# Performance work log

Measured on AMD Instinct MI355X. Metric: run time of the kernel, lower is better.

The kernel has to match this reference:

```python
import jax, jax.numpy as jnp
import numpy as np

B, C, H, W = 8, 512, 64, 64
RED = 8
D = C // RED  # query/key channels


def setup_inputs() -> dict:
    key = jax.random.key(0)
    ks = jax.random.split(key, 5)
    skip = jax.random.normal(ks[0], (B, C, H, W), dtype=jnp.float32)
    res = jax.random.normal(ks[1], (B, C, H, W), dtype=jnp.float32)
    # 1x1 Conv1d weights (no bias). Spectral norm is a weight parametrization;
    # these tensors represent the effective (normalized) weights at forward time.
    Wq = jax.random.normal(ks[2], (D, C), dtype=jnp.float32) * 0.02
    Wk = jax.random.normal(ks[3], (D, C), dtype=jnp.float32) * 0.02
    Wv = jax.random.normal(ks[4], (C, C), dtype=jnp.float32) * 0.02
    gamma = jnp.asarray([0.5], dtype=jnp.float32)  # nonzero so attention branch contributes
    return {"skip": skip, "res": res, "Wq": Wq, "Wk": Wk, "Wv": Wv, "gamma": gamma}


def reference(skip, res, Wq, Wk, Wv, gamma):
    b, c, h, w = skip.shape
    n = h * w
    x_skip = skip.reshape(b, c, n)  # [B, C, N]
    x_res = res.reshape(b, c, n)
    # 1x1 convs == per-position matmuls
    f = jnp.einsum('dc,bcn->bdn', Wq, x_skip)  # [B, D, N]
    g = jnp.einsum('dc,bcn->bdn', Wk, x_skip)  # [B, D, N]
    hv = jnp.einsum('oc,bcn->bon', Wv, x_res)  # [B, C, N]
    # scores[b, i, j] = sum_d f[b, d, i] * g[b, d, j]; softmax over dim=1 (the i axis)
    scores = jnp.einsum('bdi,bdj->bij', f, g)  # [B, N, N]
    beta = jax.nn.softmax(scores, axis=1)
    o = gamma * jnp.einsum('bci,bij->bcj', hv, beta) + x_skip  # [B, C, N]
    return o.reshape(b, c, h, w)
```

## Files before the change

kernel.cpp:

```cpp
#include <hip/hip_runtime.h>


#define B_ 8
#define C_ 512
#define N_ 4096
#define D_ 64

typedef __bf16 bf16x8 __attribute__((ext_vector_type(8)));
typedef float  f32x16 __attribute__((ext_vector_type(16)));

#define MFMA32 __builtin_amdgcn_mfma_f32_32x32x16_bf16

__device__ __forceinline__ unsigned pk_bf16(float a, float b) {
  unsigned r;
  asm("v_cvt_pk_bf16_f32 %0, %1, %2" : "=v"(r) : "v"(a), "v"(b));
  return r;
}

__device__ __forceinline__ bf16x8 ldg_frag(const unsigned short* p) {
  uint4 u = *(const uint4*)p;
  return __builtin_bit_cast(bf16x8, u);
}
__device__ __forceinline__ bf16x8 lds_frag(const unsigned char* p) {
  uint4 u = *(const uint4*)p;
  return __builtin_bit_cast(bf16x8, u);
}

__global__ void cvt_w(const float* __restrict__ src, unsigned short* __restrict__ dst, int n) {
  int i = (blockIdx.x * blockDim.x + threadIdx.x) * 2;
  if (i + 1 < n + 1) {
    unsigned v = pk_bf16(src[i], src[i + 1]);
    *(unsigned*)(dst + i) = v;
  }
}

__device__ __forceinline__ void stage64(const float* __restrict__ src,
                                        unsigned char* __restrict__ dst, int t) {
  int si = (t & 15) << 2;
  int cl = (t >> 4) << 1;
#pragma unroll
  for (int p = 0; p < 2; ++p) {
    int c = cl + p * 32;
    const float* r0 = src + (size_t)c * N_ + si;
    float4 a0 = *(const float4*)r0;
    float4 a1 = *(const float4*)(r0 + N_);
    const float* f0 = (const float*)&a0;
    const float* f1 = (const float*)&a1;
    int cb = c << 1;
#pragma unroll
    for (int k = 0; k < 4; ++k) {
      int ii = si + k;
      unsigned v = pk_bf16(f0[k], f1[k]);
      *(unsigned*)(dst + (((ii << 7) + cb) ^ ((ii & 7) << 4))) = v;
    }
  }
}

__global__ __launch_bounds__(256, 2) void fg_proj(
    const float* __restrict__ skip,
    const unsigned short* __restrict__ Wqb, const unsigned short* __restrict__ Wkb,
    unsigned short* __restrict__ Kmat, unsigned short* __restrict__ Qmat) {
  __shared__ __align__(16) unsigned char Xs[2][8192];
  int blk = blockIdx.x, b = blk & 7, i0 = (blk >> 3) << 6;
  int t = threadIdx.x, lane = t & 63, w = t >> 6, hi = lane >> 5, l5 = lane & 31;
  int dh = w >> 1, ih = w & 1;
  f32x16 ka, qa;
#pragma unroll
  for (int r = 0; r < 16; ++r) { ka[r] = 0.f; qa[r] = 0.f; }
  int il = (ih << 5) + l5;
  int dr = (dh << 5) + l5;
#pragma unroll 1
  for (int kk = 0; kk < 8; ++kk) {
    int c0 = kk << 6;
    unsigned char* buf = Xs[kk & 1];
    stage64(skip + ((size_t)(b * C_ + c0)) * N_ + i0, buf, t);
    __syncthreads();
#pragma unroll
    for (int ks = 0; ks < 4; ++ks) {
      int co = (ks << 4) + (hi << 3);
      bf16x8 aq = ldg_frag(Wqb + (size_t)dr * C_ + c0 + co);
      bf16x8 ak = ldg_frag(Wkb + (size_t)dr * C_ + c0 + co);
      bf16x8 bx = lds_frag(buf + (((il << 7) + (co << 1)) ^ ((il & 7) << 4)));
      ka = MFMA32(aq, bx, ka, 0, 0, 0);
      qa = MFMA32(ak, bx, qa, 0, 0, 0);
    }
  }
  size_t rowb = ((size_t)b * N_ + i0 + il) * D_ + (dh << 5);
#pragma unroll
  for (int q = 0; q < 4; ++q) {
    int dq = (q << 3) + (hi << 2);
    uint2 v;
    v.x = pk_bf16(ka[q * 4 + 0], ka[q * 4 + 1]);
    v.y = pk_bf16(ka[q * 4 + 2], ka[q * 4 + 3]);
    *(uint2*)(Kmat + rowb + dq) = v;
    v.x = pk_bf16(qa[q * 4 + 0], qa[q * 4 + 1]);
    v.y = pk_bf16(qa[q * 4 + 2], qa[q * 4 + 3]);
    *(uint2*)(Qmat + rowb + dq) = v;
  }
}

__global__ __launch_bounds__(256, 2) void hv_proj(
    const float* __restrict__ res, const unsigned short* __restrict__ Wvb,
    unsigned short* __restrict__ Vmat) {
  __shared__ __align__(16) unsigned char Xs[2][8192];
  int blk = blockIdx.x, b = blk & 7, i0 = (blk >> 3) << 6;
  int t = threadIdx.x, lane = t & 63, w = t >> 6, hi = lane >> 5, l5 = lane & 31;
  int cw = w << 7;
  f32x16 acc[2][4];
#pragma unroll
  for (int a = 0; a < 2; ++a)
#pragma unroll
    for (int c = 0; c < 4; ++c)
#pragma unroll
      for (int r = 0; r < 16; ++r) acc[a][c][r] = 0.f;
#pragma unroll 1
  for (int kk = 0; kk < 8; ++kk) {
    int c0 = kk << 6;
    unsigned char* buf = Xs[kk & 1];
    stage64(res + ((size_t)(b * C_ + c0)) * N_ + i0, buf, t);
    __syncthreads();
#pragma unroll
    for (int ks = 0; ks < 4; ++ks) {
      int co = (ks << 4) + (hi << 3);
      bf16x8 a0 = lds_frag(buf + (((l5 << 7) + (co << 1)) ^ ((l5 & 7) << 4)));
      bf16x8 a1 = lds_frag(buf + ((((32 + l5) << 7) + (co << 1)) ^ ((l5 & 7) << 4)));
#pragma unroll
      for (int ct = 0; ct < 4; ++ct) {
        bf16x8 bv = ldg_frag(Wvb + (size_t)(cw + (ct << 5) + l5) * C_ + c0 + co);
        acc[0][ct] = MFMA32(a0, bv, acc[0][ct], 0, 0, 0);
        acc[1][ct] = MFMA32(a1, bv, acc[1][ct], 0, 0, 0);
      }
    }
  }
#pragma unroll
  for (int ihh = 0; ihh < 2; ++ihh)
#pragma unroll
    for (int ct = 0; ct < 4; ++ct) {
      int c = cw + (ct << 5) + l5;
      unsigned short* vp = Vmat + ((size_t)b * C_ + c) * N_ + i0 + (ihh << 5);
#pragma unroll
      for (int q = 0; q < 4; ++q) {
        int iq = (q << 3) + (hi << 2);
        uint2 v;
        v.x = pk_bf16(acc[ihh][ct][q * 4 + 0], acc[ihh][ct][q * 4 + 1]);
        v.y = pk_bf16(acc[ihh][ct][q * 4 + 2], acc[ihh][ct][q * 4 + 3]);
        *(uint2*)(vp + iq) = v;
      }
    }
}

__device__ __forceinline__ void online_upd(float& m, float& l, const f32x16& s) {
  float tm = s[0];
#pragma unroll
  for (int r = 1; r < 16; ++r) tm = fmaxf(tm, s[r]);
  float nm = fmaxf(m, tm);
  float acc = l * __expf(m - nm);
#pragma unroll
  for (int r = 0; r < 16; ++r) acc += __expf(s[r] - nm);
  m = nm;
  l = acc;
}

__global__ __launch_bounds__(256) void stats_k(
    const unsigned short* __restrict__ Kmat, const unsigned short* __restrict__ Qmat,
    const float* __restrict__ gamma, float* __restrict__ m_ws, float* __restrict__ sc_ws) {
  __shared__ float mr[4][64];
  __shared__ float lr[4][64];
  int blk = blockIdx.x, b = blk & 7, j0 = (blk >> 3) << 6;
  int t = threadIdx.x, lane = t & 63, w = t >> 6, hi = lane >> 5, l5 = lane & 31;
  bf16x8 qf[2][4];
#pragma unroll
  for (int jh = 0; jh < 2; ++jh)
#pragma unroll
    for (int ks = 0; ks < 4; ++ks)
      qf[jh][ks] = ldg_frag(Qmat + ((size_t)b * N_ + j0 + (jh << 5) + l5) * D_ + (ks << 4) + (hi << 3));
  float m0 = -INFINITY, l0 = 0.f, m1 = -INFINITY, l1 = 0.f;
  for (int it = w; it < 128; it += 4) {
    const unsigned short* kp = Kmat + ((size_t)b * N_ + (it << 5) + l5) * D_ + (hi << 3);
    f32x16 s0, s1;
#pragma unroll
    for (int r = 0; r < 16; ++r) { s0[r] = 0.f; s1[r] = 0.f; }
#pragma unroll
    for (int ks = 0; ks < 4; ++ks) {
      bf16x8 a = ldg_frag(kp + (ks << 4));
      s0 = MFMA32(a, qf[0][ks], s0, 0, 0, 0);
      s1 = MFMA32(a, qf[1][ks], s1, 0, 0, 0);
    }
    online_upd(m0, l0, s0);
    online_upd(m1, l1, s1);
  }
  {
    float om = __shfl_xor(m0, 32);
    float ol = __shfl_xor(l0, 32);
    float nm = fmaxf(m0, om);
    l0 = l0 * __expf(m0 - nm) + ol * __expf(om - nm);
    m0 = nm;
    om = __shfl_xor(m1, 32);
    ol = __shfl_xor(l1, 32);
    nm = fmaxf(m1, om);
    l1 = l1 * __expf(m1 - nm) + ol * __expf(om - nm);
    m1 = nm;
  }
  mr[w][lane] = (lane < 32) ? m0 : m1;
  lr[w][lane] = (lane < 32) ? l0 : l1;
  __syncthreads();
  if (t < 64) {
    float M = mr[0][t];
#pragma unroll
    for (int ww = 1; ww < 4; ++ww) M = fmaxf(M, mr[ww][t]);
    float L = 0.f;
#pragma unroll
    for (int ww = 0; ww < 4; ++ww) L += lr[ww][t] * __expf(mr[ww][t] - M);
    m_ws[(size_t)b * N_ + j0 + t] = M;
    sc_ws[(size_t)b * N_ + j0 + t] = gamma[0] / L;
  }
}

__global__ __launch_bounds__(256, 2) void attn_pv(
    const unsigned short* __restrict__ Kmat, const unsigned short* __restrict__ Qmat,
    const unsigned short* __restrict__ Vmat, const float* __restrict__ m_ws,
    const float* __restrict__ sc_ws, const float* __restrict__ skip,
    float* __restrict__ out) {
  __shared__ __align__(16) unsigned char P[2][8192];
  int blk = blockIdx.x, b = blk & 7, j0 = (blk >> 3) << 6;
  int t = threadIdx.x, lane = t & 63, w = t >> 6, hi = lane >> 5, l5 = lane & 31;
  int ih = w >> 1, jh = w & 1, cw = w << 7;
  bf16x8 qf[4];
#pragma unroll
  for (int ks = 0; ks < 4; ++ks)
    qf[ks] = ldg_frag(Qmat + ((size_t)b * N_ + j0 + (jh << 5) + l5) * D_ + (ks << 4) + (hi << 3));
  float mj = m_ws[(size_t)b * N_ + j0 + (jh << 5) + l5];
  float scj = sc_ws[(size_t)b * N_ + j0 + (jh << 5) + l5];
  f32x16 acc[2][4];
#pragma unroll
  for (int a = 0; a < 2; ++a)
#pragma unroll
    for (int c = 0; c < 4; ++c)
#pragma unroll
      for (int r = 0; r < 16; ++r) acc[a][c][r] = 0.f;
  int jw = (jh << 5) + l5;
  unsigned wbase = jw << 7;
  unsigned wswz = (jw & 7) << 4;
#pragma unroll 1
  for (int it = 0; it < 64; ++it) {
    int ib = it << 6;
    unsigned char* pb = P[it & 1];
    const unsigned short* kp =
        Kmat + ((size_t)b * N_ + ib + (ih << 5) + l5) * D_ + (hi << 3);
    f32x16 s;
#pragma unroll
    for (int r = 0; r < 16; ++r) s[r] = 0.f;
#pragma unroll
    for (int ks = 0; ks < 4; ++ks) {
      bf16x8 a = ldg_frag(kp + (ks << 4));
      s = MFMA32(a, qf[ks], s, 0, 0, 0);
    }
#pragma unroll
    for (int pr = 0; pr < 8; ++pr) {
      float e0 = __expf(s[2 * pr] - mj) * scj;
      float e1 = __expf(s[2 * pr + 1] - mj) * scj;
      unsigned v = pk_bf16(e0, e1);
      int il = (ih << 5) + ((pr & 1) << 1) + ((pr >> 1) << 3) + (hi << 2);
      *(unsigned*)(pb + ((wbase + (il << 1)) ^ wswz)) = v;
    }
    __syncthreads();
    const unsigned short* vp = Vmat + ((size_t)b * C_ + cw + l5) * N_ + ib + (hi << 3);
#pragma unroll
    for (int ks = 0; ks < 4; ++ks) {
      int iob = ((ks << 4) + (hi << 3)) << 1;
      bf16x8 pa0 = lds_frag(pb + (((l5 << 7) + iob) ^ ((l5 & 7) << 4)));
      bf16x8 pa1 = lds_frag(pb + ((((32 + l5) << 7) + iob) ^ ((l5 & 7) << 4)));
#pragma unroll
      for (int ct = 0; ct < 4; ++ct) {
        bf16x8 bv = ldg_frag(vp + (size_t)(ct << 5) * N_ + (ks << 4));
        acc[0][ct] = MFMA32(pa0, bv, acc[0][ct], 0, 0, 0);
        acc[1][ct] = MFMA32(pa1, bv, acc[1][ct], 0, 0, 0);
      }
    }
  }
#pragma unroll
  for (int jt = 0; jt < 2; ++jt)
#pragma unroll
    for (int ct = 0; ct < 4; ++ct) {
      int c = cw + (ct << 5) + l5;
      size_t base = ((size_t)b * C_ + c) * N_ + j0 + (jt << 5) + (hi << 2);
#pragma unroll
      for (int q = 0; q < 4; ++q) {
        float4 s4 = *(const float4*)(skip + base + (q << 3));
        float4 o4;
        o4.x = acc[jt][ct][q * 4 + 0] + s4.x;
        o4.y = acc[jt][ct][q * 4 + 1] + s4.y;
        o4.z = acc[jt][ct][q * 4 + 2] + s4.z;
        o4.w = acc[jt][ct][q * 4 + 3] + s4.w;
        *(float4*)(out + base + (q << 3)) = o4;
      }
    }
}

extern "C" void kernel_launch(void* const* d_in, const int* in_sizes, int n_in,
                              void* d_out, int out_size, void* d_ws, size_t ws_size,
                              hipStream_t stream) {
  (void)in_sizes; (void)n_in; (void)out_size; (void)ws_size;
  const float* skip = (const float*)d_in[0];
  const float* res = (const float*)d_in[1];
  const float* Wq = (const float*)d_in[2];
  const float* Wk = (const float*)d_in[3];
  const float* Wv = (const float*)d_in[4];
  const float* gamma = (const float*)d_in[5];
  float* out = (float*)d_out;
  char* ws = (char*)d_ws;

  unsigned short* Kmat = (unsigned short*)(ws);
  unsigned short* Qmat = (unsigned short*)(ws + (4ull << 20));
  unsigned short* Vmat = (unsigned short*)(ws + (8ull << 20));
  float* m_ws = (float*)(ws + (40ull << 20));
  float* sc_ws = (float*)(ws + (40ull << 20) + (128ull << 10));
  unsigned short* Wqb = (unsigned short*)(ws + (40ull << 20) + (256ull << 10));
  unsigned short* Wkb = Wqb + 64 * 512;
  unsigned short* Wvb = Wkb + 64 * 512;

  cvt_w<<<64, 256, 0, stream>>>(Wq, Wqb, 64 * 512);
  cvt_w<<<64, 256, 0, stream>>>(Wk, Wkb, 64 * 512);
  cvt_w<<<512, 256, 0, stream>>>(Wv, Wvb, 512 * 512);
  fg_proj<<<512, 256, 0, stream>>>(skip, Wqb, Wkb, Kmat, Qmat);
  hv_proj<<<512, 256, 0, stream>>>(res, Wvb, Vmat);
  stats_k<<<512, 256, 0, stream>>>(Kmat, Qmat, gamma, m_ws, sc_ws);
  attn_pv<<<512, 256, 0, stream>>>(Kmat, Qmat, Vmat, m_ws, sc_ws, skip, out);
}
```

Measured before the change: 605.6 us.

## Split attention over channel halves, prefetch V fragments, widen stats kernel

attn_pv now launches twice as many blocks, each covering half of the channel dimension (64 channels per wave instead of 128). This halves the accumulator registers so occupancy can rise to 3 blocks per SIMD, and V fragments are loaded at the top of each iteration so the loads overlap the score MFMA and exp work. The cost is that QK^T scores and the exp are recomputed twice per j-tile. stats_k moves to 512 threads with 8 waves, and the online softmax update uses tree max reductions and two partial sums for more ILP. P stores are widened to 8-byte writes.

```diff
diff --git a/kernel.cpp b/kernel.cpp
--- a/kernel.cpp
+++ b/kernel.cpp
@@ -150,22 +150,28 @@
 }
 
 __device__ __forceinline__ void online_upd(float& m, float& l, const f32x16& s) {
-  float tm = s[0];
-#pragma unroll
-  for (int r = 1; r < 16; ++r) tm = fmaxf(tm, s[r]);
+  float t0 = fmaxf(s[0], s[1]),  t1 = fmaxf(s[2], s[3]);
+  float t2 = fmaxf(s[4], s[5]),  t3 = fmaxf(s[6], s[7]);
+  float t4 = fmaxf(s[8], s[9]),  t5 = fmaxf(s[10], s[11]);
+  float t6 = fmaxf(s[12], s[13]), t7 = fmaxf(s[14], s[15]);
+  t0 = fmaxf(t0, t1); t2 = fmaxf(t2, t3); t4 = fmaxf(t4, t5); t6 = fmaxf(t6, t7);
+  float tm = fmaxf(fmaxf(t0, t2), fmaxf(t4, t6));
   float nm = fmaxf(m, tm);
-  float acc = l * __expf(m - nm);
-#pragma unroll
-  for (int r = 0; r < 16; ++r) acc += __expf(s[r] - nm);
+  float a0 = l * __expf(m - nm), a1 = 0.f;
+#pragma unroll
+  for (int r = 0; r < 16; r += 2) {
+    a0 += __expf(s[r] - nm);
+    a1 += __expf(s[r + 1] - nm);
+  }
   m = nm;
-  l = acc;
-}
-
-__global__ __launch_bounds__(256) void stats_k(
+  l = a0 + a1;
+}
+
+__global__ __launch_bounds__(512) void stats_k(
     const unsigned short* __restrict__ Kmat, const unsigned short* __restrict__ Qmat,
     const float* __restrict__ gamma, float* __restrict__ m_ws, float* __restrict__ sc_ws) {
-  __shared__ float mr[4][64];
-  __shared__ float lr[4][64];
+  __shared__ float mr[8][64];
+  __shared__ float lr[8][64];
   int blk = blockIdx.x, b = blk & 7, j0 = (blk >> 3) << 6;
   int t = threadIdx.x, lane = t & 63, w = t >> 6, hi = lane >> 5, l5 = lane & 31;
   bf16x8 qf[2][4];
@@ -175,7 +181,7 @@
     for (int ks = 0; ks < 4; ++ks)
       qf[jh][ks] = ldg_frag(Qmat + ((size_t)b * N_ + j0 + (jh << 5) + l5) * D_ + (ks << 4) + (hi << 3));
   float m0 = -INFINITY, l0 = 0.f, m1 = -INFINITY, l1 = 0.f;
-  for (int it = w; it < 128; it += 4) {
+  for (int it = w; it < 128; it += 8) {
     const unsigned short* kp = Kmat + ((size_t)b * N_ + (it << 5) + l5) * D_ + (hi << 3);
     f32x16 s0, s1;
 #pragma unroll
@@ -207,46 +213,54 @@
   if (t < 64) {
     float M = mr[0][t];
 #pragma unroll
-    for (int ww = 1; ww < 4; ++ww) M = fmaxf(M, mr[ww][t]);
+    for (int ww = 1; ww < 8; ++ww) M = fmaxf(M, mr[ww][t]);
     float L = 0.f;
 #pragma unroll
-    for (int ww = 0; ww < 4; ++ww) L += lr[ww][t] * __expf(mr[ww][t] - M);
+    for (int ww = 0; ww < 8; ++ww) L += lr[ww][t] * __expf(mr[ww][t] - M);
     m_ws[(size_t)b * N_ + j0 + t] = M;
     sc_ws[(size_t)b * N_ + j0 + t] = gamma[0] / L;
   }
 }
 
-__global__ __launch_bounds__(256, 2) void attn_pv(
+__global__ __launch_bounds__(256, 3) void attn_pv(
     const unsigned short* __restrict__ Kmat, const unsigned short* __restrict__ Qmat,
     const unsigned short* __restrict__ Vmat, const float* __restrict__ m_ws,
     const float* __restrict__ sc_ws, const float* __restrict__ skip,
     float* __restrict__ out) {
   __shared__ __align__(16) unsigned char P[2][8192];
-  int blk = blockIdx.x, b = blk & 7, j0 = (blk >> 3) << 6;
+  int blk = blockIdx.x, b = blk & 7, ch = (blk >> 3) & 1, j0 = (blk >> 4) << 6;
   int t = threadIdx.x, lane = t & 63, w = t >> 6, hi = lane >> 5, l5 = lane & 31;
-  int ih = w >> 1, jh = w & 1, cw = w << 7;
+  int ih = w >> 1, jh = w & 1;
+  int cbase = (ch << 8) + (w << 6);
   bf16x8 qf[4];
 #pragma unroll
   for (int ks = 0; ks < 4; ++ks)
     qf[ks] = ldg_frag(Qmat + ((size_t)b * N_ + j0 + (jh << 5) + l5) * D_ + (ks << 4) + (hi << 3));
   float mj = m_ws[(size_t)b * N_ + j0 + (jh << 5) + l5];
   float scj = sc_ws[(size_t)b * N_ + j0 + (jh << 5) + l5];
-  f32x16 acc[2][4];
+  f32x16 acc[2][2];
 #pragma unroll
   for (int a = 0; a < 2; ++a)
 #pragma unroll
-    for (int c = 0; c < 4; ++c)
+    for (int c = 0; c < 2; ++c)
 #pragma unroll
       for (int r = 0; r < 16; ++r) acc[a][c][r] = 0.f;
   int jw = (jh << 5) + l5;
   unsigned wbase = jw << 7;
   unsigned wswz = (jw & 7) << 4;
+  const unsigned short* Vb = Vmat + ((size_t)b * C_ + cbase + l5) * N_ + (hi << 3);
+  const unsigned short* Kb = Kmat + ((size_t)b * N_ + (ih << 5) + l5) * D_ + (hi << 3);
 #pragma unroll 1
   for (int it = 0; it < 64; ++it) {
     int ib = it << 6;
     unsigned char* pb = P[it & 1];
-    const unsigned short* kp =
-        Kmat + ((size_t)b * N_ + ib + (ih << 5) + l5) * D_ + (hi << 3);
+    bf16x8 vf[2][4];
+#pragma unroll
+    for (int ct = 0; ct < 2; ++ct)
+#pragma unroll
+      for (int ks = 0; ks < 4; ++ks)
+        vf[ct][ks] = ldg_frag(Vb + (size_t)(ct << 5) * N_ + ib + (ks << 4));
+    const unsigned short* kp = Kb + (size_t)ib * D_;
     f32x16 s;
 #pragma unroll
     for (int r = 0; r < 16; ++r) s[r] = 0.f;
@@ -256,33 +270,35 @@
       s = MFMA32(a, qf[ks], s, 0, 0, 0);
     }
 #pragma unroll
-    for (int pr = 0; pr < 8; ++pr) {
-      float e0 = __expf(s[2 * pr] - mj) * scj;
-      float e1 = __expf(s[2 * pr + 1] - mj) * scj;
-      unsigned v = pk_bf16(e0, e1);
-      int il = (ih << 5) + ((pr & 1) << 1) + ((pr >> 1) << 3) + (hi << 2);
-      *(unsigned*)(pb + ((wbase + (il << 1)) ^ wswz)) = v;
+    for (int q = 0; q < 4; ++q) {
+      float e0 = __expf(s[4 * q + 0] - mj) * scj;
+      float e1 = __expf(s[4 * q + 1] - mj) * scj;
+      float e2 = __expf(s[4 * q + 2] - mj) * scj;
+      float e3 = __expf(s[4 * q + 3] - mj) * scj;
+      uint2 v;
+      v.x = pk_bf16(e0, e1);
+      v.y = pk_bf16(e2, e3);
+      int il = (ih << 5) + (q << 3) + (hi << 2);
+      *(uint2*)(pb + ((wbase + (il << 1)) ^ wswz)) = v;
     }
     __syncthreads();
-    const unsigned short* vp = Vmat + ((size_t)b * C_ + cw + l5) * N_ + ib + (hi << 3);
 #pragma unroll
     for (int ks = 0; ks < 4; ++ks) {
       int iob = ((ks << 4) + (hi << 3)) << 1;
       bf16x8 pa0 = lds_frag(pb + (((l5 << 7) + iob) ^ ((l5 & 7) << 4)));
       bf16x8 pa1 = lds_frag(pb + ((((32 + l5) << 7) + iob) ^ ((l5 & 7) << 4)));
 #pragma unroll
-      for (int ct = 0; ct < 4; ++ct) {
-        bf16x8 bv = ldg_frag(vp + (size_t)(ct << 5) * N_ + (ks << 4));
-        acc[0][ct] = MFMA32(pa0, bv, acc[0][ct], 0, 0, 0);
-        acc[1][ct] = MFMA32(pa1, bv, acc[1][ct], 0, 0, 0);
+      for (int ct = 0; ct < 2; ++ct) {
+        acc[0][ct] = MFMA32(pa0, vf[ct][ks], acc[0][ct], 0, 0, 0);
+        acc[1][ct] = MFMA32(pa1, vf[ct][ks], acc[1][ct], 0, 0, 0);
       }
     }
   }
 #pragma unroll
   for (int jt = 0; jt < 2; ++jt)
 #pragma unroll
-    for (int ct = 0; ct < 4; ++ct) {
-      int c = cw + (ct << 5) + l5;
+    for (int ct = 0; ct < 2; ++ct) {
+      int c = cbase + (ct << 5) + l5;
       size_t base = ((size_t)b * C_ + c) * N_ + j0 + (jt << 5) + (hi << 2);
 #pragma unroll
       for (int q = 0; q < 4; ++q) {
@@ -324,6 +340,6 @@
   cvt_w<<<512, 256, 0, stream>>>(Wv, Wvb, 512 * 512);
   fg_proj<<<512, 256, 0, stream>>>(skip, Wqb, Wkb, Kmat, Qmat);
   hv_proj<<<512, 256, 0, stream>>>(res, Wvb, Vmat);
-  stats_k<<<512, 256, 0, stream>>>(Kmat, Qmat, gamma, m_ws, sc_ws);
-  attn_pv<<<512, 256, 0, stream>>>(Kmat, Qmat, Vmat, m_ws, sc_ws, skip, out);
-}
+  stats_k<<<512, 512, 0, stream>>>(Kmat, Qmat, gamma, m_ws, sc_ws);
+  attn_pv<<<1024, 256, 0, stream>>>(Kmat, Qmat, Vmat, m_ws, sc_ws, skip, out);
+}
```

Measured after the change: 619.4 us. 2.3% more time.
